# Optimization experiments

Hardware: AMD Instinct MI355X
Metric: run time of the kernel (lower is better)

The kernel has to match this reference:

```python
import jax, jax.numpy as jnp
import numpy as np

NUM_HEADS = 8

def setup_inputs() -> dict:
    key = jax.random.key(0)
    k1, k2, k3, k4 = jax.random.split(key, 4)
    B, N, S, C = 16, 256, 4096, 512
    return {
        "query": jax.random.normal(k1, (B, N, C), dtype=jnp.float32),
        "key": jax.random.normal(k2, (B, S, C), dtype=jnp.float32),
        "Wq": jax.random.normal(k3, (C, C), dtype=jnp.float32) * (C ** -0.5),
        "Wk": jax.random.normal(k4, (C, C), dtype=jnp.float32) * (C ** -0.5),
    }

def reference(query, key, Wq, Wk):
    B, N, C = query.shape
    S = key.shape[1]
    H = NUM_HEADS
    hd = C // H
    scale = hd ** -0.5
    # value = key (v_proj is Identity, value defaults to key)
    q = (query @ Wq).reshape(B, N, H, hd)   # b n h c
    k = (key @ Wk).reshape(B, S, H, hd)     # b s h c
    raw_attn = jnp.einsum('bnhc,bshc->bhns', q, k) * scale  # [B,H,N,S]
    # softmax over the QUERY axis (dim=-2), non-standard
    attn = jax.nn.softmax(raw_attn, axis=-2)
    # clamp-normalize over token axis; divisor is detached in the original
    div = jnp.clip(jnp.sum(attn, axis=-1, keepdims=True), 1.0, None)
    attn = attn / jax.lax.stop_gradient(div)
    # attn_drop has p=0.0 -> identity
    v = key.reshape(B, S, H, hd)
    out = jnp.einsum('bhns,bshc->bnhc', attn, v).reshape(B, N, C)
    # out_style = attn @ key_heads; since value == key this equals out
    out_style = out
    return out, out_style
```

## Files before the change

kernel.cpp:

```cpp
#include <hip/hip_runtime.h>
#include <hip/hip_bf16.h>


typedef __attribute__((ext_vector_type(8))) short bf16x8;
typedef __attribute__((ext_vector_type(4))) float f32x4;
typedef unsigned int u32;

__device__ __forceinline__ unsigned short f2bf(float f) {
  union { __hip_bfloat16 h; unsigned short u; } cv;
  cv.h = __float2bfloat16(f);
  return cv.u;
}

__device__ __forceinline__ u32 pkbf(float a, float b) {
  union { __hip_bfloat162 h; u32 u; } cv;
  cv.h = __float22bfloat162_rn(float2{a, b});
  return cv.u;
}

__device__ __forceinline__ void async_copy16(const void* gptr, void* lptr) {
  __builtin_amdgcn_global_load_lds((const __attribute__((address_space(1))) u32*)gptr,
                                   (__attribute__((address_space(3))) u32*)lptr,
                                   16, 0, 0);
}

__global__ __launch_bounds__(256) void prep_w(const float* __restrict__ Wq,
                                              const float* __restrict__ Wk,
                                              unsigned short* __restrict__ WtQ,
                                              unsigned short* __restrict__ WtK) {
  __shared__ float tile[64][65];
  const int blk = blockIdx.x;
  const float* W = (blk & 1) ? Wk : Wq;
  unsigned short* Wt = (blk & 1) ? WtK : WtQ;
  const int tb = blk >> 1;
  const int k0 = (tb >> 3) * 64, n0 = (tb & 7) * 64;
  const int t = threadIdx.x;
  const int row = t >> 4, col4 = (t & 15) * 4;
#pragma unroll
  for (int i = 0; i < 4; ++i) {
    int r = i * 16 + row;
    float4 v = *reinterpret_cast<const float4*>(&W[(size_t)(k0 + r) * 512 + n0 + col4]);
    tile[r][col4 + 0] = v.x; tile[r][col4 + 1] = v.y;
    tile[r][col4 + 2] = v.z; tile[r][col4 + 3] = v.w;
  }
  __syncthreads();
#pragma unroll
  for (int i = 0; i < 4; ++i) {
    int r = i * 16 + row;
    short4 s;
    s.x = (short)f2bf(tile[col4 + 0][r]);
    s.y = (short)f2bf(tile[col4 + 1][r]);
    s.z = (short)f2bf(tile[col4 + 2][r]);
    s.w = (short)f2bf(tile[col4 + 3][r]);
    *reinterpret_cast<short4*>(&Wt[(size_t)(n0 + r) * 512 + k0 + col4]) = s;
  }
}

__global__ __launch_bounds__(256, 2) void gemm_xw(const float* __restrict__ Xk,
                                                  const unsigned short* __restrict__ WtKp,
                                                  __hip_bfloat16* __restrict__ Yk,
                                                  const float* __restrict__ Xq,
                                                  const unsigned short* __restrict__ WtQp,
                                                  __hip_bfloat16* __restrict__ Yq) {
  __shared__ unsigned short As[2][128 * 64];
  __shared__ unsigned short Bs[2][128 * 64];
  const int t = threadIdx.x;
  const int wave = t >> 6, lane = t & 63, l15 = lane & 15, quad = lane >> 4;

  const int nwg = gridDim.x * gridDim.y;
  const int d = blockIdx.y * gridDim.x + blockIdx.x;
  const int tile = (d & 7) * (nwg >> 3) + (d >> 3);

  const float* X; const unsigned short* Wt; __hip_bfloat16* Y; int n0, m0;
  if (tile < 2048) { X = Xk; Wt = WtKp; Y = Yk; n0 = (tile & 3) * 128; m0 = (tile >> 2) * 128; }
  else { int u = tile - 2048; X = Xq; Wt = WtQp; Y = Yq; n0 = (u & 3) * 128; m0 = (u >> 2) * 128; }

  const int wm = (wave >> 1) * 64, wn = (wave & 1) * 64;
  const int b_rl = lane >> 3;
  const int b_cs = (lane & 7) ^ b_rl;
  const int cr = t >> 3, cc = t & 7;

  f32x4 acc[4][4];
#pragma unroll
  for (int i = 0; i < 4; ++i)
#pragma unroll
    for (int j = 0; j < 4; ++j) { f32x4 z = {0.f, 0.f, 0.f, 0.f}; acc[i][j] = z; }

  float4 fA[2][4][2];

#define ISSUE_B(kt) do {                                                             \
    const int S_ = (kt) & 1; const int kk_ = (kt) * 64;                              \
    const unsigned short* bB_ = Wt + (size_t)n0 * 512 + kk_;                         \
    _Pragma("unroll")                                                                \
    for (int o_ = 0; o_ < 4; ++o_) {                                                 \
      int rg_ = wave * 4 + o_;                                                       \
      async_copy16(bB_ + (size_t)(rg_ * 8 + b_rl) * 512 + b_cs * 8,                  \
                   &Bs[S_][rg_ * 512]);                                              \
    }                                                                                \
  } while (0)

#define ISSUE_A(kt) do {                                                             \
    const int S_ = (kt) & 1; const int kk_ = (kt) * 64;                              \
    const float* aB_ = X + (size_t)m0 * 512 + kk_;                                   \
    _Pragma("unroll")                                                                \
    for (int i_ = 0; i_ < 4; ++i_) {                                                 \
      const float* p_ = aB_ + (size_t)(i_ * 32 + cr) * 512 + cc * 8;                 \
      fA[S_][i_][0] = *reinterpret_cast<const float4*>(p_);                          \
      fA[S_][i_][1] = *reinterpret_cast<const float4*>(p_ + 4);                      \
    }                                                                                \
  } while (0)

#define CVT_PUB(kt) do {                                                             \
    const int S_ = (kt) & 1;                                                         \
    _Pragma("unroll")                                                                \
    for (int i_ = 0; i_ < 4; ++i_) {                                                 \
      uint4 w_;                                                                      \
      w_.x = pkbf(fA[S_][i_][0].x, fA[S_][i_][0].y);                                 \
      w_.y = pkbf(fA[S_][i_][0].z, fA[S_][i_][0].w);                                 \
      w_.z = pkbf(fA[S_][i_][1].x, fA[S_][i_][1].y);                                 \
      w_.w = pkbf(fA[S_][i_][1].z, fA[S_][i_][1].w);                                 \
      int r_ = i_ * 32 + cr;                                                         \
      *reinterpret_cast<uint4*>(&As[S_][r_ * 64 + ((cc ^ (r_ & 7)) << 3)]) = w_;     \
    }                                                                                \
  } while (0)

#define COMPUTE(kt) do {                                                             \
    const int S_ = (kt) & 1;                                                         \
    _Pragma("unroll")                                                                \
    for (int x_ = 0; x_ < 2; ++x_) {                                                 \
      bf16x8 a_[4], b_[4];                                                           \
      _Pragma("unroll")                                                              \
      for (int i_ = 0; i_ < 4; ++i_) {                                               \
        int ra_ = wm + 16 * i_ + l15;                                                \
        a_[i_] = *reinterpret_cast<const bf16x8*>(                                   \
            &As[S_][ra_ * 64 + (((x_ * 4 + quad) ^ (ra_ & 7)) << 3)]);               \
      }                                                                              \
      _Pragma("unroll")                                                              \
      for (int j_ = 0; j_ < 4; ++j_) {                                               \
        int rb_ = wn + 16 * j_ + l15;                                                \
        b_[j_] = *reinterpret_cast<const bf16x8*>(                                   \
            &Bs[S_][rb_ * 64 + (((x_ * 4 + quad) ^ (rb_ & 7)) << 3)]);               \
      }                                                                              \
      _Pragma("unroll")                                                              \
      for (int i_ = 0; i_ < 4; ++i_)                                                 \
        _Pragma("unroll")                                                            \
        for (int j_ = 0; j_ < 4; ++j_)                                               \
          acc[i_][j_] =                                                              \
              __builtin_amdgcn_mfma_f32_16x16x32_bf16(a_[i_], b_[j_], acc[i_][j_],   \
                                                      0, 0, 0);                      \
    }                                                                                \
  } while (0)

  ISSUE_B(0);
  __builtin_amdgcn_sched_barrier(0);
  ISSUE_A(0);
  __builtin_amdgcn_sched_barrier(0);
  ISSUE_A(1);
  __builtin_amdgcn_sched_barrier(0);
  CVT_PUB(0);
  asm volatile("s_waitcnt vmcnt(8)" ::: "memory");
  asm volatile("s_waitcnt lgkmcnt(0)" ::: "memory");
  __builtin_amdgcn_sched_barrier(0);
  __builtin_amdgcn_s_barrier();
  __builtin_amdgcn_sched_barrier(0);

#pragma unroll
  for (int it = 0; it < 8; ++it) {
    if (it < 7) { ISSUE_B(it + 1); __builtin_amdgcn_sched_barrier(0); }
    if (it < 6) { ISSUE_A(it + 2); __builtin_amdgcn_sched_barrier(0); }

    COMPUTE(it);

    if (it < 7) {
      CVT_PUB(it + 1);
      if (it < 6) asm volatile("s_waitcnt vmcnt(8)" ::: "memory");
      else        asm volatile("s_waitcnt vmcnt(0)" ::: "memory");
      asm volatile("s_waitcnt lgkmcnt(0)" ::: "memory");
      __builtin_amdgcn_sched_barrier(0);
      __builtin_amdgcn_s_barrier();
      __builtin_amdgcn_sched_barrier(0);
    }
  }

#undef ISSUE_B
#undef ISSUE_A
#undef CVT_PUB
#undef COMPUTE

#pragma unroll
  for (int i = 0; i < 4; ++i)
#pragma unroll
    for (int j = 0; j < 4; ++j)
#pragma unroll
      for (int r = 0; r < 4; ++r) {
        int m = m0 + wm + 16 * i + 4 * quad + r;
        int n = n0 + wn + 16 * j + l15;
        Y[(size_t)m * 512 + n] = __float2bfloat16(acc[i][j][r]);
      }
}

__global__ __launch_bounds__(512, 2) void attn_kernel(const __hip_bfloat16* __restrict__ qg,
                                                      const __hip_bfloat16* __restrict__ kg,
                                                      const float* __restrict__ keyg,
                                                      float* __restrict__ accg,
                                                      float* __restrict__ rsg) {
  __shared__ unsigned short qs[256 * 64];
  __shared__ unsigned short vs[64 * 128];
  __shared__ unsigned short pst[256 * 128];

  const int t = threadIdx.x;
  const int wave = t >> 6, lane = t & 63, l15 = lane & 15, quad = lane >> 4;
  const int blk = blockIdx.x, chunk = blk & 1, bh = blk >> 1, b = bh >> 3, h = bh & 7;
  const int l7 = l15 & 7;

  {
    const unsigned short* qbase = (const unsigned short*)qg + (size_t)(b * 256) * 512 + h * 64;
#pragma unroll
    for (int i = 0; i < 4; ++i) {
      int lin = i * 512 + t;
      int n = lin >> 3, cc = lin & 7, phys = cc ^ (n & 7);
      bf16x8 v = *reinterpret_cast<const bf16x8*>(qbase + (size_t)n * 512 + cc * 8);
      *reinterpret_cast<bf16x8*>(&qs[n * 64 + phys * 8]) = v;
    }
  }

  const unsigned short* kbase = (const unsigned short*)kg + (size_t)(b * 4096 + chunk * 2048) * 512 + h * 64;
  const float* vbase = keyg + (size_t)(b * 4096 + chunk * 2048) * 512 + h * 64;

  bf16x8 kc0 = *reinterpret_cast<const bf16x8*>(kbase + (size_t)(16 * wave + l15) * 512 + quad * 8);
  bf16x8 kc1 = *reinterpret_cast<const bf16x8*>(kbase + (size_t)(16 * wave + l15) * 512 + 32 + quad * 8);
  float vbuf[16];
#pragma unroll
  for (int half = 0; half < 2; ++half) {
    int sc = wave + 8 * half;
#pragma unroll
    for (int j = 0; j < 8; ++j)
      vbuf[half * 8 + j] = vbase[(size_t)(sc * 8 + j) * 512 + lane];
  }

  union { bf16x8 f; int w[4]; } ones_u;
  ones_u.w[0] = 0x3F803F80; ones_u.w[1] = 0x3F803F80;
  ones_u.w[2] = 0x3F803F80; ones_u.w[3] = 0x3F803F80;
  const bf16x8 ones = ones_u.f;

  f32x4 oacc[2][4], rsacc[2];
#pragma unroll
  for (int i = 0; i < 2; ++i) {
    f32x4 z = {0.f, 0.f, 0.f, 0.f};
    rsacc[i] = z;
#pragma unroll
    for (int j = 0; j < 4; ++j) oacc[i][j] = z;
  }

  __syncthreads();

  for (int it = 0; it < 16; ++it) {
    f32x4 L[16];
#pragma unroll
    for (int jt = 0; jt < 16; ++jt) { f32x4 z = {0.f, 0.f, 0.f, 0.f}; L[jt] = z; }
#pragma unroll
    for (int x = 0; x < 2; ++x) {
      bf16x8 kf = x ? kc1 : kc0;
#pragma unroll
      for (int jt = 0; jt < 16; ++jt) {
        bf16x8 bq = *reinterpret_cast<const bf16x8*>(
            &qs[(16 * jt + l15) * 64 + ((4 * x + quad) ^ l7) * 8]);
        L[jt] = __builtin_amdgcn_mfma_f32_16x16x32_bf16(kf, bq, L[jt], 0, 0, 0);
      }
    }

    const int nit = (it < 15) ? it + 1 : 15;
    kc0 = *reinterpret_cast<const bf16x8*>(kbase + (size_t)(nit * 128 + 16 * wave + l15) * 512 + quad * 8);
    kc1 = *reinterpret_cast<const bf16x8*>(kbase + (size_t)(nit * 128 + 16 * wave + l15) * 512 + 32 + quad * 8);

    float cs0 = 0.f, cs1 = 0.f, cs2 = 0.f, cs3 = 0.f;
#pragma unroll
    for (int jt = 0; jt < 16; ++jt) {
      float e0 = __expf(L[jt][0] * 0.125f);
      float e1 = __expf(L[jt][1] * 0.125f);
      float e2 = __expf(L[jt][2] * 0.125f);
      float e3 = __expf(L[jt][3] * 0.125f);
      L[jt][0] = e0; L[jt][1] = e1; L[jt][2] = e2; L[jt][3] = e3;
      cs0 += e0; cs1 += e1; cs2 += e2; cs3 += e3;
    }
#pragma unroll
    for (int m = 1; m <= 8; m <<= 1) {
      cs0 += __shfl_xor(cs0, m);
      cs1 += __shfl_xor(cs1, m);
      cs2 += __shfl_xor(cs2, m);
      cs3 += __shfl_xor(cs3, m);
    }
    const float ri0 = 1.0f / cs0, ri1 = 1.0f / cs1, ri2 = 1.0f / cs2, ri3 = 1.0f / cs3;

    __syncthreads();

#pragma unroll
    for (int half = 0; half < 2; ++half) {
      int sc = wave + 8 * half;
      uint4 w;
      w.x = pkbf(vbuf[half * 8 + 0], vbuf[half * 8 + 1]);
      w.y = pkbf(vbuf[half * 8 + 2], vbuf[half * 8 + 3]);
      w.z = pkbf(vbuf[half * 8 + 4], vbuf[half * 8 + 5]);
      w.w = pkbf(vbuf[half * 8 + 6], vbuf[half * 8 + 7]);
      *reinterpret_cast<uint4*>(&vs[lane * 128 + (sc ^ (lane & 7)) * 8]) = w;
    }

    {
      const int scw = 2 * wave + (quad >> 1);
      const int half8 = (quad & 1) * 4;
#pragma unroll
      for (int jt = 0; jt < 16; ++jt) {
        uint2 w;
        w.x = pkbf(L[jt][0] * ri0, L[jt][1] * ri1);
        w.y = pkbf(L[jt][2] * ri2, L[jt][3] * ri3);
        int row = 16 * jt + l15;
        *reinterpret_cast<uint2*>(&pst[row * 128 + ((scw ^ l7) * 8) + half8]) = w;
      }
    }

    __syncthreads();

#pragma unroll
    for (int half = 0; half < 2; ++half) {
      int sc = wave + 8 * half;
#pragma unroll
      for (int j = 0; j < 8; ++j)
        vbuf[half * 8 + j] = vbase[(size_t)(nit * 128 + sc * 8 + j) * 512 + lane];
    }

#pragma unroll
    for (int kc = 0; kc < 4; ++kc) {
      bf16x8 bv[4];
#pragma unroll
      for (int jc = 0; jc < 4; ++jc)
        bv[jc] = *reinterpret_cast<const bf16x8*>(
            &vs[(16 * jc + l15) * 128 + ((4 * kc + quad) ^ l7) * 8]);
#pragma unroll
      for (int jtl = 0; jtl < 2; ++jtl) {
        int rowp = 16 * (2 * wave + jtl) + l15;
        bf16x8 ap = *reinterpret_cast<const bf16x8*>(
            &pst[rowp * 128 + ((4 * kc + quad) ^ l7) * 8]);
#pragma unroll
        for (int jc = 0; jc < 4; ++jc)
          oacc[jtl][jc] = __builtin_amdgcn_mfma_f32_16x16x32_bf16(ap, bv[jc], oacc[jtl][jc], 0, 0, 0);
        rsacc[jtl] = __builtin_amdgcn_mfma_f32_16x16x32_bf16(ap, ones, rsacc[jtl], 0, 0, 0);
      }
    }
  }

  float* rsp = rsg + chunk * 32768 + bh * 256;
  if (l15 == 0) {
#pragma unroll
    for (int jtl = 0; jtl < 2; ++jtl)
#pragma unroll
      for (int r = 0; r < 4; ++r)
        rsp[16 * (2 * wave + jtl) + 4 * quad + r] = rsacc[jtl][r];
  }
  float* ap_ = accg + (size_t)chunk * 2097152 + (size_t)bh * 16384;
#pragma unroll
  for (int jtl = 0; jtl < 2; ++jtl)
#pragma unroll
    for (int jc = 0; jc < 4; ++jc)
#pragma unroll
      for (int r = 0; r < 4; ++r)
        ap_[(16 * (2 * wave + jtl) + 4 * quad + r) * 64 + 16 * jc + l15] = oacc[jtl][jc][r];
}

__global__ __launch_bounds__(256) void finalize(const float* __restrict__ acc,
                                                const float* __restrict__ rs,
                                                float* __restrict__ out) {
  int g = blockIdx.x * 256 + threadIdx.x;
  int c = (g & 15) * 4, n = (g >> 4) & 255, bh = g >> 12;
  int e = g * 4;
  float4 v0 = *reinterpret_cast<const float4*>(&acc[e]);
  float4 v1 = *reinterpret_cast<const float4*>(&acc[e + 2097152]);
  float r = rs[bh * 256 + n] + rs[32768 + bh * 256 + n];
  float inv = 1.0f / fmaxf(r, 1.0f);
  float4 o;
  o.x = (v0.x + v1.x) * inv; o.y = (v0.y + v1.y) * inv;
  o.z = (v0.z + v1.z) * inv; o.w = (v0.w + v1.w) * inv;
  int b = bh >> 3, h = bh & 7;
  size_t oi = ((size_t)(b * 256 + n)) * 512 + h * 64 + c;
  *reinterpret_cast<float4*>(&out[oi]) = o;
  *reinterpret_cast<float4*>(&out[oi + 2097152]) = o;
}

extern "C" void kernel_launch(void* const* d_in, const int* in_sizes, int n_in,
                              void* d_out, int out_size, void* d_ws, size_t ws_size,
                              hipStream_t stream) {
  const float* query = (const float*)d_in[0];
  const float* key   = (const float*)d_in[1];
  const float* Wq    = (const float*)d_in[2];
  const float* Wk    = (const float*)d_in[3];
  float* out = (float*)d_out;
  char* ws = (char*)d_ws;

  unsigned short* WtQ = (unsigned short*)(ws);
  unsigned short* WtK = (unsigned short*)(ws + 524288);
  __hip_bfloat16* qbf = (__hip_bfloat16*)(ws + 1048576);
  __hip_bfloat16* kbf = (__hip_bfloat16*)(ws + 5242880);
  float* accw = (float*)(ws + 72351744);
  float* rsw  = (float*)(ws + 89128960);

  prep_w<<<128, 256, 0, stream>>>(Wq, Wk, WtQ, WtK);
  gemm_xw<<<dim3(4, 544), 256, 0, stream>>>(key, WtK, kbf, query, WtQ, qbf);
  attn_kernel<<<256, 512, 0, stream>>>(qbf, kbf, key, accw, rsw);
  finalize<<<2048, 256, 0, stream>>>(accw, rsw, out);
}
```

Before: 320.6 us.

## Pre-cast key and query to bf16 once and reuse for GEMM and values

Extends the weight-prep kernel with extra blocks that convert the fp32 key and query tensors to bf16 in a workspace buffer. A new GEMM kernel reads these bf16 inputs with async global-to-LDS copies instead of converting fp32 inside the GEMM. The attention kernel then loads bf16 values from the cast buffer instead of fp32 key, halving the value-load bytes. The cost is an extra full read-and-write pass over key (about 128MB in plus 64MB out), and the new path only runs when the workspace is large enough.

```diff
diff --git a/kernel.cpp b/kernel.cpp
--- a/kernel.cpp
+++ b/kernel.cpp
@@ -27,14 +27,30 @@
 __global__ __launch_bounds__(256) void prep_w(const float* __restrict__ Wq,
                                               const float* __restrict__ Wk,
                                               unsigned short* __restrict__ WtQ,
-                                              unsigned short* __restrict__ WtK) {
+                                              unsigned short* __restrict__ WtK,
+                                              const float* __restrict__ key,
+                                              unsigned short* __restrict__ kcast,
+                                              const float* __restrict__ query,
+                                              unsigned short* __restrict__ qcast) {
   __shared__ float tile[64][65];
   const int blk = blockIdx.x;
+  const int t = threadIdx.x;
+  if (blk >= 128) {
+    const float* src; unsigned short* dst; size_t idx;
+    if (blk < 128 + 16384) { src = key;   dst = kcast; idx = ((size_t)(blk - 128) * 256 + t) * 8; }
+    else                   { src = query; dst = qcast; idx = ((size_t)(blk - 16512) * 256 + t) * 8; }
+    float4 u = *reinterpret_cast<const float4*>(&src[idx]);
+    float4 v = *reinterpret_cast<const float4*>(&src[idx + 4]);
+    uint4 w;
+    w.x = pkbf(u.x, u.y); w.y = pkbf(u.z, u.w);
+    w.z = pkbf(v.x, v.y); w.w = pkbf(v.z, v.w);
+    *reinterpret_cast<uint4*>(&dst[idx]) = w;
+    return;
+  }
   const float* W = (blk & 1) ? Wk : Wq;
   unsigned short* Wt = (blk & 1) ? WtK : WtQ;
   const int tb = blk >> 1;
   const int k0 = (tb >> 3) * 64, n0 = (tb & 7) * 64;
-  const int t = threadIdx.x;
   const int row = t >> 4, col4 = (t & 15) * 4;
 #pragma unroll
   for (int i = 0; i < 4; ++i) {
@@ -54,6 +70,92 @@
     s.w = (short)f2bf(tile[col4 + 3][r]);
     *reinterpret_cast<short4*>(&Wt[(size_t)(n0 + r) * 512 + k0 + col4]) = s;
   }
+}
+
+__global__ __launch_bounds__(256, 2) void gemm_bb(const unsigned short* __restrict__ Ak,
+                                                  const unsigned short* __restrict__ WtKp,
+                                                  __hip_bfloat16* __restrict__ Yk,
+                                                  const unsigned short* __restrict__ Aq,
+                                                  const unsigned short* __restrict__ WtQp,
+                                                  __hip_bfloat16* __restrict__ Yq) {
+  __shared__ unsigned short As[2][128 * 64];
+  __shared__ unsigned short Bs[2][128 * 64];
+  const int t = threadIdx.x;
+  const int wave = t >> 6, lane = t & 63, l15 = lane & 15, quad = lane >> 4;
+
+  const int nwg = gridDim.x * gridDim.y;
+  const int d = blockIdx.y * gridDim.x + blockIdx.x;
+  const int tile = (d & 7) * (nwg >> 3) + (d >> 3);
+
+  const unsigned short* A; const unsigned short* Wt; __hip_bfloat16* Y; int n0, m0;
+  if (tile < 2048) { A = Ak; Wt = WtKp; Y = Yk; n0 = (tile & 3) * 128; m0 = (tile >> 2) * 128; }
+  else { int u = tile - 2048; A = Aq; Wt = WtQp; Y = Yq; n0 = (u & 3) * 128; m0 = (u >> 2) * 128; }
+
+  const int wm = (wave >> 1) * 64, wn = (wave & 1) * 64;
+  const int rl = lane >> 3;
+  const int cs = (lane & 7) ^ rl;
+
+  const unsigned short* Abase = A + (size_t)m0 * 512;
+  const unsigned short* Bbase = Wt + (size_t)n0 * 512;
+
+  f32x4 acc[4][4];
+#pragma unroll
+  for (int i = 0; i < 4; ++i)
+#pragma unroll
+    for (int j = 0; j < 4; ++j) { f32x4 z = {0.f, 0.f, 0.f, 0.f}; acc[i][j] = z; }
+
+#define STAGE_BB(kt, S_) do {                                                        \
+    const unsigned short* aB_ = Abase + (kt) * 64;                                   \
+    const unsigned short* bB_ = Bbase + (kt) * 64;                                   \
+    _Pragma("unroll")                                                                \
+    for (int o_ = 0; o_ < 4; ++o_) {                                                 \
+      int rg_ = wave * 4 + o_;                                                       \
+      async_copy16(aB_ + (size_t)(rg_ * 8 + rl) * 512 + cs * 8, &As[S_][rg_ * 512]); \
+      async_copy16(bB_ + (size_t)(rg_ * 8 + rl) * 512 + cs * 8, &Bs[S_][rg_ * 512]); \
+    }                                                                                \
+  } while (0)
+
+  STAGE_BB(0, 0);
+
+#pragma unroll 2
+  for (int it = 0; it < 8; ++it) {
+    const int S = it & 1;
+    __syncthreads();
+    if (it < 7) STAGE_BB(it + 1, S ^ 1);
+    __builtin_amdgcn_sched_barrier(0);
+
+#pragma unroll
+    for (int x = 0; x < 2; ++x) {
+      bf16x8 a[4], bfr[4];
+#pragma unroll
+      for (int i = 0; i < 4; ++i) {
+        int ra = wm + 16 * i + l15;
+        a[i] = *reinterpret_cast<const bf16x8*>(&As[S][ra * 64 + (((x * 4 + quad) ^ (ra & 7)) << 3)]);
+      }
+#pragma unroll
+      for (int j = 0; j < 4; ++j) {
+        int rb = wn + 16 * j + l15;
+        bfr[j] = *reinterpret_cast<const bf16x8*>(&Bs[S][rb * 64 + (((x * 4 + quad) ^ (rb & 7)) << 3)]);
+      }
+#pragma unroll
+      for (int i = 0; i < 4; ++i)
+#pragma unroll
+        for (int j = 0; j < 4; ++j)
+          acc[i][j] = __builtin_amdgcn_mfma_f32_16x16x32_bf16(a[i], bfr[j], acc[i][j], 0, 0, 0);
+    }
+  }
+#undef STAGE_BB
+
+#pragma unroll
+  for (int i = 0; i < 4; ++i)
+#pragma unroll
+    for (int j = 0; j < 4; ++j)
+#pragma unroll
+      for (int r = 0; r < 4; ++r) {
+        int m = m0 + wm + 16 * i + 4 * quad + r;
+        int n = n0 + wn + 16 * j + l15;
+        Y[(size_t)m * 512 + n] = __float2bfloat16(acc[i][j][r]);
+      }
 }
 
 __global__ __launch_bounds__(256, 2) void gemm_xw(const float* __restrict__ Xk,
@@ -199,9 +301,11 @@
       }
 }
 
+template<bool USEBF>
 __global__ __launch_bounds__(512, 2) void attn_kernel(const __hip_bfloat16* __restrict__ qg,
                                                       const __hip_bfloat16* __restrict__ kg,
                                                       const float* __restrict__ keyg,
+                                                      const unsigned short* __restrict__ vcast,
                                                       float* __restrict__ accg,
                                                       float* __restrict__ rsg) {
   __shared__ unsigned short qs[256 * 64];
@@ -226,16 +330,20 @@
 
   const unsigned short* kbase = (const unsigned short*)kg + (size_t)(b * 4096 + chunk * 2048) * 512 + h * 64;
   const float* vbase = keyg + (size_t)(b * 4096 + chunk * 2048) * 512 + h * 64;
+  const unsigned short* vbase_h = vcast + (size_t)(b * 4096 + chunk * 2048) * 512 + h * 64;
 
   bf16x8 kc0 = *reinterpret_cast<const bf16x8*>(kbase + (size_t)(16 * wave + l15) * 512 + quad * 8);
   bf16x8 kc1 = *reinterpret_cast<const bf16x8*>(kbase + (size_t)(16 * wave + l15) * 512 + 32 + quad * 8);
-  float vbuf[16];
+  float vf[16];
+  unsigned short vh[16];
 #pragma unroll
   for (int half = 0; half < 2; ++half) {
     int sc = wave + 8 * half;
 #pragma unroll
-    for (int j = 0; j < 8; ++j)
-      vbuf[half * 8 + j] = vbase[(size_t)(sc * 8 + j) * 512 + lane];
+    for (int j = 0; j < 8; ++j) {
+      if constexpr (USEBF) vh[half * 8 + j] = vbase_h[(size_t)(sc * 8 + j) * 512 + lane];
+      else                 vf[half * 8 + j] = vbase[(size_t)(sc * 8 + j) * 512 + lane];
+    }
   }
 
   union { bf16x8 f; int w[4]; } ones_u;
@@ -298,10 +406,17 @@
     for (int half = 0; half < 2; ++half) {
       int sc = wave + 8 * half;
       uint4 w;
-      w.x = pkbf(vbuf[half * 8 + 0], vbuf[half * 8 + 1]);
-      w.y = pkbf(vbuf[half * 8 + 2], vbuf[half * 8 + 3]);
-      w.z = pkbf(vbuf[half * 8 + 4], vbuf[half * 8 + 5]);
-      w.w = pkbf(vbuf[half * 8 + 6], vbuf[half * 8 + 7]);
+      if constexpr (USEBF) {
+        w.x = (u32)vh[half * 8 + 0] | ((u32)vh[half * 8 + 1] << 16);
+        w.y = (u32)vh[half * 8 + 2] | ((u32)vh[half * 8 + 3] << 16);
+        w.z = (u32)vh[half * 8 + 4] | ((u32)vh[half * 8 + 5] << 16);
+        w.w = (u32)vh[half * 8 + 6] | ((u32)vh[half * 8 + 7] << 16);
+      } else {
+        w.x = pkbf(vf[half * 8 + 0], vf[half * 8 + 1]);
+        w.y = pkbf(vf[half * 8 + 2], vf[half * 8 + 3]);
+        w.z = pkbf(vf[half * 8 + 4], vf[half * 8 + 5]);
+        w.w = pkbf(vf[half * 8 + 6], vf[half * 8 + 7]);
+      }
       *reinterpret_cast<uint4*>(&vs[lane * 128 + (sc ^ (lane & 7)) * 8]) = w;
     }
 
@@ -324,8 +439,10 @@
     for (int half = 0; half < 2; ++half) {
       int sc = wave + 8 * half;
 #pragma unroll
-      for (int j = 0; j < 8; ++j)
-        vbuf[half * 8 + j] = vbase[(size_t)(nit * 128 + sc * 8 + j) * 512 + lane];
+      for (int j = 0; j < 8; ++j) {
+        if constexpr (USEBF) vh[half * 8 + j] = vbase_h[(size_t)(nit * 128 + sc * 8 + j) * 512 + lane];
+        else                 vf[half * 8 + j] = vbase[(size_t)(nit * 128 + sc * 8 + j) * 512 + lane];
+      }
     }
 
 #pragma unroll
@@ -401,9 +518,18 @@
   __hip_bfloat16* kbf = (__hip_bfloat16*)(ws + 5242880);
   float* accw = (float*)(ws + 72351744);
   float* rsw  = (float*)(ws + 89128960);
-
-  prep_w<<<128, 256, 0, stream>>>(Wq, Wk, WtQ, WtK);
-  gemm_xw<<<dim3(4, 544), 256, 0, stream>>>(key, WtK, kbf, query, WtQ, qbf);
-  attn_kernel<<<256, 512, 0, stream>>>(qbf, kbf, key, accw, rsw);
+  unsigned short* kcast = (unsigned short*)(ws + 89391104);
+  unsigned short* qcast = (unsigned short*)(ws + 156499968);
+  const bool usebf = ws_size >= 160694272ull;
+
+  if (usebf) {
+    prep_w<<<17536, 256, 0, stream>>>(Wq, Wk, WtQ, WtK, key, kcast, query, qcast);
+    gemm_bb<<<dim3(4, 544), 256, 0, stream>>>(kcast, WtK, kbf, qcast, WtQ, qbf);
+    attn_kernel<true><<<256, 512, 0, stream>>>(qbf, kbf, key, kcast, accw, rsw);
+  } else {
+    prep_w<<<128, 256, 0, stream>>>(Wq, Wk, WtQ, WtK, key, nullptr, query, nullptr);
+    gemm_xw<<<dim3(4, 544), 256, 0, stream>>>(key, WtK, kbf, query, WtQ, qbf);
+    attn_kernel<false><<<256, 512, 0, stream>>>(qbf, kbf, key, nullptr, accw, rsw);
+  }
   finalize<<<2048, 256, 0, stream>>>(accw, rsw, out);
 }
```

Result: slower. 331.0 us (+3.3%).
